# Performance work log

Hardware: AMD Instinct MI355X
Metric: run time of the kernel (lower is better)

The kernel has to match this reference:

```python
import jax, jax.numpy as jnp
import numpy as np

A = -0.75  # PyTorch bicubic convolution constant

def _cubic_weights(t):
    # t: fractional part in [0,1). Returns the 4 tap weights
    # (matches PyTorch get_cubic_upsample_coefficients with A=-0.75).
    t1 = t + 1.0
    w0 = ((A * t1 - 5.0 * A) * t1 + 8.0 * A) * t1 - 4.0 * A
    w1 = ((A + 2.0) * t - (A + 3.0)) * t * t + 1.0
    s = 1.0 - t
    w2 = ((A + 2.0) * s - (A + 3.0)) * s * s + 1.0
    s2 = 2.0 - t
    w3 = ((A * s2 - 5.0 * A) * s2 + 8.0 * A) * s2 - 4.0 * A
    return (w0, w1, w2, w3)

def _reflect_index(i, size):
    # integer reflection for padding_mode='reflection', align_corners=True over [0, size-1]
    span = size - 1
    if span <= 0:
        return jnp.zeros_like(i)
    m = jnp.abs(i) % (2 * span)
    return jnp.where(m > span, 2 * span - m, m)

def _bicubic_warp(x, flow):
    # x: [B,C,H,W], flow: [B,2,H,W] (flow[:,0]=dx, flow[:,1]=dy)
    B, C, H, W = x.shape
    gx = jnp.arange(W, dtype=x.dtype)
    gy = jnp.arange(H, dtype=x.dtype)
    # normalize-to-[-1,1] then grid_sample unnormalize (align_corners=True) cancel exactly:
    ix = gx[None, None, :] + flow[:, 0]  # [B,H,W] source x coord
    iy = gy[None, :, None] + flow[:, 1]  # [B,H,W] source y coord
    bx = jnp.floor(ix)
    by = jnp.floor(iy)
    tx = ix - bx
    ty = iy - by
    bx = bx.astype(jnp.int32)
    by = by.astype(jnp.int32)
    wx = _cubic_weights(tx)
    wy = _cubic_weights(ty)
    xf = x.reshape(B, C, H * W)
    out = jnp.zeros_like(x)
    for j in range(4):  # fixed 4x4 tap stencil
        Y = _reflect_index(by + (j - 1), H)
        for i in range(4):
            X = _reflect_index(bx + (i - 1), W)
            idx = (Y * W + X).reshape(B, 1, H * W)
            v = jnp.take_along_axis(xf, idx, axis=2).reshape(B, C, H, W)
            out = out + v * (wy[j] * wx[i])[:, None]
    return out

def setup_inputs() -> dict:
    key = jax.random.key(0)
    k1, k2, k3 = jax.random.split(key, 3)
    B, C, H, W = 8, 4, 1024, 1024
    return {
        "input": jax.random.normal(k1, (B, C, H, W), dtype=jnp.float32),
        "target": jax.random.normal(k2, (B, C, H, W), dtype=jnp.float32),
        "flow": jax.random.normal(k3, (B, 2, H, W), dtype=jnp.float32),
    }

def reference(input, target, flow):
    warped = _bicubic_warp(target, flow)
    b = 5
    return jnp.mean(jnp.abs(input[..., b:-b, b:-b] - warped[..., b:-b, b:-b]))
```

## Files before the change

kernel.cpp:

```cpp
#include <hip/hip_runtime.h>

constexpr int BB = 8, CC = 4, HH = 1024, WW = 1024, CROP = 5;
constexpr int HC = HH - 2 * CROP, WC = WW - 2 * CROP;
constexpr int HW = HH * WW;
constexpr float AA = -0.75f;

constexpr int NSTRIP = 16;
constexpr int GRID = 32 * NSTRIP * 2;
constexpr int RING = 16;
constexpr int SWID = 272;
constexpr int CH_STRIDE = RING * SWID;

typedef __attribute__((address_space(1))) const void gv_t;
typedef __attribute__((address_space(3))) void lv_t;

__device__ __forceinline__ int reflect_small(int i) {
    int r = i < 0 ? -i : i;
    return r > (HH - 1) ? 2 * (HH - 1) - r : r;
}

__device__ __forceinline__ void cubic_w(float t, float& w0, float& w1,
                                        float& w2, float& w3) {
    float t1 = t + 1.0f;
    w0 = ((AA * t1 - 5.0f * AA) * t1 + 8.0f * AA) * t1 - 4.0f * AA;
    w1 = ((AA + 2.0f) * t - (AA + 3.0f)) * t * t + 1.0f;
    float s = 1.0f - t;
    w2 = ((AA + 2.0f) * s - (AA + 3.0f)) * s * s + 1.0f;
    float s2 = 2.0f - t;
    w3 = ((AA * s2 - 5.0f * AA) * s2 + 8.0f * AA) * s2 - 4.0f * AA;
}

__device__ __noinline__ float px_slow2(const float* __restrict__ tgt_p,
                                       const float* __restrict__ in_p, int pix,
                                       int bx, int by, float wx0, float wx1,
                                       float wx2, float wx3, float wy0,
                                       float wy1, float wy2, float wy3) {
    const int r0 = reflect_small(by - 1) * WW;
    const int r1 = reflect_small(by) * WW;
    const int r2 = reflect_small(by + 1) * WW;
    const int r3 = reflect_small(by + 2) * WW;
    const int c0 = reflect_small(bx - 1);
    const int c1 = reflect_small(bx);
    const int c2 = reflect_small(bx + 1);
    const int c3 = reflect_small(bx + 2);
    float acc = 0.0f;
#pragma unroll
    for (int c = 0; c < 2; ++c) {
        const float* tb = tgt_p + c * HW;
        float q0 = wx0 * tb[r0 + c0] + wx1 * tb[r0 + c1] + wx2 * tb[r0 + c2] +
                   wx3 * tb[r0 + c3];
        float q1 = wx0 * tb[r1 + c0] + wx1 * tb[r1 + c1] + wx2 * tb[r1 + c2] +
                   wx3 * tb[r1 + c3];
        float q2 = wx0 * tb[r2 + c0] + wx1 * tb[r2 + c1] + wx2 * tb[r2 + c2] +
                   wx3 * tb[r2 + c3];
        float q3 = wx0 * tb[r3 + c0] + wx1 * tb[r3 + c1] + wx2 * tb[r3 + c2] +
                   wx3 * tb[r3 + c3];
        float v = wy0 * q0 + wy1 * q1 + wy2 * q2 + wy3 * q3;
        acc += fabsf(in_p[c * HW + pix] - v);
    }
    return acc;
}

__global__ __launch_bounds__(256, 4) void warp_loss_k(
    const float* __restrict__ input, const float* __restrict__ target,
    const float* __restrict__ flow, float* __restrict__ wsbuf) {
    __shared__ float cache[2 * CH_STRIDE];
    const int tid = (int)threadIdx.x;
    const int wv = tid >> 6, lane = tid & 63;

    const int low = (int)blockIdx.x & 511;
    const int pair = (int)blockIdx.x >> 9;
    const int colid = low >> 4;
    const int strip = low & 15;
    const int b = colid >> 2;
    const int chunk = colid & 3;
    const int x0 = CROP + chunk * 256;
    const int wscol = chunk == 0 ? 0 : chunk == 1 ? 252 : chunk == 2 ? 508 : 752;
    const int y0 = CROP + strip * 64;
    const int y1 = min(y0 + 64, CROP + HC);

    const int x = x0 + tid;
    const bool valid_px = x <= 1018;
    const int xc = valid_px ? x : 1018;

    const float* tgt_p = target + (size_t)b * CC * HW + (size_t)(pair * 2) * HW;
    const float* in_p = input + (size_t)b * CC * HW + (size_t)(pair * 2) * HW;
    const float* flow_b = flow + (size_t)b * 2 * HW;

    const int chv = wv >> 1, part = wv & 1;
    const float* plane = tgt_p + (size_t)chv * HW;
    const int chbase = chv * CH_STRIDE;

#pragma unroll 1
    for (int k = 0; k < 11; ++k) {
        const int r = y0 - 5 + k;
        const int slot = r & (RING - 1);
        const float* src = plane + (size_t)r * WW + wscol;
        if (part == 0) {
            __builtin_amdgcn_global_load_lds(
                (gv_t*)(src + lane * 4), (lv_t*)&cache[chbase + slot * SWID],
                16, 0, 0);
        } else {
            __builtin_amdgcn_global_load_lds(
                (gv_t*)(src + 208 + lane),
                (lv_t*)&cache[chbase + slot * SWID + 208], 4, 0, 0);
        }
    }

    {
        const int p0 = y0 * WW + xc;
    }
    float dxn = flow_b[y0 * WW + xc];
    float dyn = flow_b[HW + y0 * WW + xc];
    float i0n = in_p[y0 * WW + xc];
    float i1n = in_p[HW + y0 * WW + xc];

    __syncthreads();

    float lsum = 0.0f;

    for (int y = y0; y < y1; ++y) {
        const float dx = dxn, dy = dyn;
        const float i0v = i0n, i1v = i1n;

        {
            const int yn = (y + 1 < y1) ? y + 1 : y;
            const int pixn = yn * WW + xc;
            dxn = flow_b[pixn];
            dyn = flow_b[HW + pixn];
            i0n = in_p[pixn];
            i1n = in_p[HW + pixn];
        }

        {
            const int r = y + 6;
            if (r < HH) {
                const int slot = r & (RING - 1);
                const float* src = plane + (size_t)r * WW + wscol;
                if (part == 0) {
                    __builtin_amdgcn_global_load_lds(
                        (gv_t*)(src + lane * 4),
                        (lv_t*)&cache[chbase + slot * SWID], 16, 0, 0);
                } else {
                    __builtin_amdgcn_global_load_lds(
                        (gv_t*)(src + 208 + lane),
                        (lv_t*)&cache[chbase + slot * SWID + 208], 4, 0, 0);
                }
            }
        }

        const int pix = y * WW + xc;
        const float fx = (float)xc + dx;
        const float fy = (float)y + dy;
        const float bxf = floorf(fx), byf = floorf(fy);
        const int bx = (int)bxf, by = (int)byf;
        const float tx = fx - bxf, ty = fy - byf;

        float wx0, wx1, wx2, wx3, wy0, wy1, wy2, wy3;
        cubic_w(tx, wx0, wx1, wx2, wx3);
        cubic_w(ty, wy0, wy1, wy2, wy3);

        const int d = by - y;
        const int cx = bx - 1 - wscol;
        const bool fast =
            valid_px & (d >= -4) & (d <= 3) & (cx >= 0) & (cx <= 268);

        if (fast) {
            const int t = (by - 1) & (RING - 1);
            float v0 = 0.0f, v1 = 0.0f;
#pragma unroll
            for (int j = 0; j < 4; ++j) {
                const int s = (t + j) & (RING - 1);
                const int base = s * SWID + cx;
                const float wyj =
                    j == 0 ? wy0 : j == 1 ? wy1 : j == 2 ? wy2 : wy3;
                const float* p0 = &cache[base];
                const float* p1 = &cache[CH_STRIDE + base];
                v0 += wyj * (p0[0] * wx0 + p0[1] * wx1 + p0[2] * wx2 + p0[3] * wx3);
                v1 += wyj * (p1[0] * wx0 + p1[1] * wx1 + p1[2] * wx2 + p1[3] * wx3);
            }
            lsum += fabsf(i0v - v0) + fabsf(i1v - v1);
        } else if (valid_px) {
            lsum += px_slow2(tgt_p, in_p, pix, bx, by, wx0, wx1, wx2, wx3,
                             wy0, wy1, wy2, wy3);
        }

        __syncthreads();
    }

#pragma unroll
    for (int off2 = 32; off2 > 0; off2 >>= 1) lsum += __shfl_down(lsum, off2);

    __shared__ float sm[4];
    if (lane == 0) sm[wv] = lsum;
    __syncthreads();
    if (tid == 0) wsbuf[blockIdx.x] = sm[0] + sm[1] + sm[2] + sm[3];
}

__global__ __launch_bounds__(1024) void reduce_k(const float* __restrict__ ws,
                                                 float* __restrict__ out) {
    float s = 0.0f;
    for (int i = threadIdx.x; i < GRID; i += 1024) s += ws[i];
#pragma unroll
    for (int off = 32; off > 0; off >>= 1) s += __shfl_down(s, off);
    __shared__ float sm[16];
    const int lane = threadIdx.x & 63;
    const int wv = threadIdx.x >> 6;
    if (lane == 0) sm[wv] = s;
    __syncthreads();
    if (threadIdx.x == 0) {
        float t = 0.0f;
#pragma unroll
        for (int i = 0; i < 16; ++i) t += sm[i];
        constexpr float inv_count = 1.0f / ((float)BB * CC * HC * WC);
        out[0] = t * inv_count;
    }
}

extern "C" void kernel_launch(void* const* d_in, const int* in_sizes, int n_in,
                              void* d_out, int out_size, void* d_ws,
                              size_t ws_size, hipStream_t stream) {
    const float* input = (const float*)d_in[0];
    const float* target = (const float*)d_in[1];
    const float* flow = (const float*)d_in[2];
    float* ws = (float*)d_ws;
    float* out = (float*)d_out;

    warp_loss_k<<<GRID, 256, 0, stream>>>(input, target, flow, ws);
    reduce_k<<<1, 1024, 0, stream>>>(ws, out);
}
```

Measured before the change: 118.1 us.

## Store target tile in LDS as packed fp16 pairs with shifted duplicate layout

The target row cache in LDS now holds packed half2 values. Each row is stored twice: once as even-aligned pairs and once as pairs shifted by one element. A 4-tap horizontal read then becomes two aligned dword loads instead of four float loads. Rows are staged through registers with ordinary vector global loads and converted to fp16, replacing the asynchronous global-to-LDS copies. The converted values are written after the compute step, before the barrier. This aims to cut LDS read traffic and bank pressure in the gather loop, at the cost of fp16 rounding of the target samples, extra conversion ALU work and more live registers.

Result: slower. 142.7 us (+20.9%).

```diff
diff --git a/kernel.cpp b/kernel.cpp
--- a/kernel.cpp
+++ b/kernel.cpp
@@ -1,4 +1,5 @@
 #include <hip/hip_runtime.h>
+#include <hip/hip_fp16.h>
 
 constexpr int BB = 8, CC = 4, HH = 1024, WW = 1024, CROP = 5;
 constexpr int HC = HH - 2 * CROP, WC = WW - 2 * CROP;
@@ -11,8 +12,8 @@
 constexpr int SWID = 272;
 constexpr int CH_STRIDE = RING * SWID;
 
-typedef __attribute__((address_space(1))) const void gv_t;
-typedef __attribute__((address_space(3))) void lv_t;
+typedef float f4 __attribute__((ext_vector_type(4)));
+typedef f4 uf4 __attribute__((aligned(4)));
 
 __device__ __forceinline__ int reflect_small(int i) {
     int r = i < 0 ? -i : i;
@@ -61,10 +62,15 @@
     return acc;
 }
 
+__device__ __forceinline__ unsigned pk(float a, float b) {
+    __half2 h = __floats2half2_rn(a, b);
+    return __builtin_bit_cast(unsigned, h);
+}
+
 __global__ __launch_bounds__(256, 4) void warp_loss_k(
     const float* __restrict__ input, const float* __restrict__ target,
     const float* __restrict__ flow, float* __restrict__ wsbuf) {
-    __shared__ float cache[2 * CH_STRIDE];
+    __shared__ unsigned cacheU[2 * CH_STRIDE];
     const int tid = (int)threadIdx.x;
     const int wv = tid >> 6, lane = tid & 63;
 
@@ -87,29 +93,36 @@
     const float* in_p = input + (size_t)b * CC * HW + (size_t)(pair * 2) * HW;
     const float* flow_b = flow + (size_t)b * 2 * HW;
 
-    const int chv = wv >> 1, part = wv & 1;
+    const int chv = wv >> 1, q = wv & 1;
     const float* plane = tgt_p + (size_t)chv * HW;
     const int chbase = chv * CH_STRIDE;
+    const int k1 = lane + q * 64;
+    const bool has_k2 = (q == 0) && (lane < 8);
+    const int k2 = lane + 128;
 
 #pragma unroll 1
-    for (int k = 0; k < 11; ++k) {
-        const int r = y0 - 5 + k;
-        const int slot = r & (RING - 1);
+    for (int kk = 0; kk < 11; ++kk) {
+        const int r = y0 - 5 + kk;
+        const int sb = chbase + (r & (RING - 1)) * SWID;
         const float* src = plane + (size_t)r * WW + wscol;
-        if (part == 0) {
-            __builtin_amdgcn_global_load_lds(
-                (gv_t*)(src + lane * 4), (lv_t*)&cache[chbase + slot * SWID],
-                16, 0, 0);
-        } else {
-            __builtin_amdgcn_global_load_lds(
-                (gv_t*)(src + 208 + lane),
-                (lv_t*)&cache[chbase + slot * SWID + 208], 4, 0, 0);
-        }
-    }
-
-    {
-        const int p0 = y0 * WW + xc;
-    }
+        {
+            f4 g = *(const uf4*)(src + 2 * k1);
+            cacheU[sb + k1] = pk(g.x, g.y);
+            cacheU[sb + 136 + k1] = pk(g.y, g.z);
+        }
+        if (has_k2) {
+            if (k2 < 135) {
+                f4 g = *(const uf4*)(src + 2 * k2);
+                cacheU[sb + k2] = pk(g.x, g.y);
+                cacheU[sb + 136 + k2] = pk(g.y, g.z);
+            } else {
+                float2 g = *(const float2*)(src + 270);
+                cacheU[sb + 135] = pk(g.x, g.y);
+                cacheU[sb + 136 + 135] = pk(g.y, 0.0f);
+            }
+        }
+    }
+
     float dxn = flow_b[y0 * WW + xc];
     float dyn = flow_b[HW + y0 * WW + xc];
     float i0n = in_p[y0 * WW + xc];
@@ -123,6 +136,19 @@
         const float dx = dxn, dy = dyn;
         const float i0v = i0n, i1v = i1n;
 
+        const int r = y + 6;
+        const bool do_stage = r < HH;
+        f4 g1 = {0, 0, 0, 0};
+        float2 g2l = {0, 0};
+        f4 g2 = {0, 0, 0, 0};
+        if (do_stage) {
+            const float* src = plane + (size_t)r * WW + wscol;
+            g1 = *(const uf4*)(src + 2 * k1);
+            if (has_k2) {
+                if (k2 < 135) g2 = *(const uf4*)(src + 2 * k2);
+                else g2l = *(const float2*)(src + 270);
+            }
+        }
         {
             const int yn = (y + 1 < y1) ? y + 1 : y;
             const int pixn = yn * WW + xc;
@@ -132,23 +158,6 @@
             i1n = in_p[HW + pixn];
         }
 
-        {
-            const int r = y + 6;
-            if (r < HH) {
-                const int slot = r & (RING - 1);
-                const float* src = plane + (size_t)r * WW + wscol;
-                if (part == 0) {
-                    __builtin_amdgcn_global_load_lds(
-                        (gv_t*)(src + lane * 4),
-                        (lv_t*)&cache[chbase + slot * SWID], 16, 0, 0);
-                } else {
-                    __builtin_amdgcn_global_load_lds(
-                        (gv_t*)(src + 208 + lane),
-                        (lv_t*)&cache[chbase + slot * SWID + 208], 4, 0, 0);
-                }
-            }
-        }
-
         const int pix = y * WW + xc;
         const float fx = (float)xc + dx;
         const float fy = (float)y + dy;
@@ -166,23 +175,49 @@
             valid_px & (d >= -4) & (d <= 3) & (cx >= 0) & (cx <= 268);
 
         if (fast) {
-            const int t = (by - 1) & (RING - 1);
+            const int idx = (cx >> 1) + ((cx & 1) * 136);
+            const int t0 = (by - 1) & (RING - 1);
             float v0 = 0.0f, v1 = 0.0f;
 #pragma unroll
             for (int j = 0; j < 4; ++j) {
-                const int s = (t + j) & (RING - 1);
-                const int base = s * SWID + cx;
+                const int s = (t0 + j) & (RING - 1);
+                const int a0 = s * SWID + idx;
                 const float wyj =
                     j == 0 ? wy0 : j == 1 ? wy1 : j == 2 ? wy2 : wy3;
-                const float* p0 = &cache[base];
-                const float* p1 = &cache[CH_STRIDE + base];
-                v0 += wyj * (p0[0] * wx0 + p0[1] * wx1 + p0[2] * wx2 + p0[3] * wx3);
-                v1 += wyj * (p1[0] * wx0 + p1[1] * wx1 + p1[2] * wx2 + p1[3] * wx3);
+                {
+                    unsigned d0 = cacheU[a0];
+                    unsigned d1 = cacheU[a0 + 1];
+                    float2 f0 = __half22float2(__builtin_bit_cast(__half2, d0));
+                    float2 f1 = __half22float2(__builtin_bit_cast(__half2, d1));
+                    v0 += wyj * (f0.x * wx0 + f0.y * wx1 + f1.x * wx2 + f1.y * wx3);
+                }
+                {
+                    unsigned d0 = cacheU[CH_STRIDE + a0];
+                    unsigned d1 = cacheU[CH_STRIDE + a0 + 1];
+                    float2 f0 = __half22float2(__builtin_bit_cast(__half2, d0));
+                    float2 f1 = __half22float2(__builtin_bit_cast(__half2, d1));
+                    v1 += wyj * (f0.x * wx0 + f0.y * wx1 + f1.x * wx2 + f1.y * wx3);
+                }
             }
             lsum += fabsf(i0v - v0) + fabsf(i1v - v1);
         } else if (valid_px) {
             lsum += px_slow2(tgt_p, in_p, pix, bx, by, wx0, wx1, wx2, wx3,
                              wy0, wy1, wy2, wy3);
+        }
+
+        if (do_stage) {
+            const int sb = chbase + (r & (RING - 1)) * SWID;
+            cacheU[sb + k1] = pk(g1.x, g1.y);
+            cacheU[sb + 136 + k1] = pk(g1.y, g1.z);
+            if (has_k2) {
+                if (k2 < 135) {
+                    cacheU[sb + k2] = pk(g2.x, g2.y);
+                    cacheU[sb + 136 + k2] = pk(g2.y, g2.z);
+                } else {
+                    cacheU[sb + 135] = pk(g2l.x, g2l.y);
+                    cacheU[sb + 136 + 135] = pk(g2l.y, 0.0f);
+                }
+            }
         }
 
         __syncthreads();
```
